# Kernel optimization log

Hardware: AMD Instinct MI355X
Metric: run time of the kernel (lower is better)

The kernel has to match this reference:

```python
import jax, jax.numpy as jnp
import numpy as np

THETA = 1.0
DILATIONS = (1, 2, 3, 4)
EPS = 1e-6


def _scale_features(x, d):
    # x: [B, C, H, W]; one pyramid scale (dilation d)
    B, C, H, W = x.shape
    k = 3 + 2 * (d - 1)          # kernel size per original formula
    pad = d * d                   # pad so effective span d*(k-1)+1 = 2d^2+1 preserves HxW
    K = k * k
    patches = jax.lax.conv_general_dilated_patches(
        x, (k, k), (1, 1), [(pad, pad), (pad, pad)], rhs_dilation=(d, d)
    )  # [B, C*K, H, W], channel-major per input channel
    p = patches.reshape(B, C, K, H, W)

    mu = p.mean(axis=2, keepdims=True)
    diff = p - mu
    var_biased = (diff * diff).mean(axis=2)                 # E[(p-mu)^2]
    std = jnp.sqrt(var_biased * (K / (K - 1))) + EPS        # torch .std is unbiased (ddof=1)

    contrast = var_biased / (std * std)                     # mean(normed^2)
    energy = (p * p).mean(axis=2)
    entropy = -(p * jnp.log(p + EPS)).mean(axis=2)
    # NB: original precedence -> 1.0 / mean(1 + |p - mu|)
    homogeneity = 1.0 / ((1.0 + jnp.abs(diff)).mean(axis=2))

    feats = jnp.stack([contrast, energy, entropy, homogeneity], axis=2)  # [B, C, 4, H, W]
    # martingale transform: exp(theta*log(f+eps) - 0.5*theta^2)
    M = jnp.exp(THETA * jnp.log(feats + EPS) - 0.5 * THETA ** 2)
    return M.reshape(B, C * 4, H, W)  # cat over channels of per-channel feature stacks


def setup_inputs() -> dict:
    key = jax.random.key(0)
    x = jax.random.uniform(key, (2, 4, 256, 256), dtype=jnp.float32)
    return {"x": x}


def reference(x):
    return tuple(_scale_features(x, d) for d in DILATIONS)
```

## Files before the change

### kernel.cpp

```cpp
#include <hip/hip_runtime.h>
#include <cstddef>

#define EPS 1e-6f
constexpr float INV_SQRT_E = 0.6065306597126334f;

template <int D>
__device__ __forceinline__ void body(const float* __restrict__ x,
                                     float* __restrict__ out,
                                     char* smem, int bc, int H, int W)
{
    constexpr int PAD = D * D;
    constexpr int KS  = 2 * D + 1;
    constexpr int K   = KS * KS;
    constexpr int TW  = 64, TH = 8;
    constexpr int LW  = TW + 2 * PAD;
    constexpr int LH  = TH + 2 * PAD;
    constexpr int NE  = LH * LW;
    constexpr int NI  = (NE + 511) / 512;
    constexpr float INVK = 1.0f / (float)K;
    constexpr float UNB  = (float)K / (float)(K - 1);

    float2* sv  = (float2*)smem;
    float2* cs2 = (float2*)(smem + LH * LW * 8);
    float*  cs1 = (float*) (smem + LH * LW * 8 + TH * LW * 8);

    const int w0 = blockIdx.x * TW;
    const int h0 = blockIdx.y * TH;
    const float* xp = x + (size_t)bc * H * W;
    const int tid = threadIdx.y * 64 + threadIdx.x;

    float vb[NI];
    #pragma unroll
    for (int i = 0; i < NI; ++i) {
        const int idx = tid + i * 512;
        float v = 0.0f;
        if (idx < NE) {
            const int r  = idx / LW;
            const int cc = idx - r * LW;
            const int gh = h0 - PAD + r;
            const int gw = w0 - PAD + cc;
            if (gh >= 0 && gh < H && gw >= 0 && gw < W) v = xp[gh * W + gw];
        }
        vb[i] = v;
    }
    #pragma unroll
    for (int i = 0; i < NI; ++i) {
        const int idx = tid + i * 512;
        if (idx < NE)
            sv[idx] = make_float2(vb[i], vb[i] * __logf(vb[i] + EPS));
    }
    __syncthreads();

    const int tx = threadIdx.x;
    const int ty = threadIdx.y;

    float s = 0.0f, s2 = 0.0f, sl = 0.0f;
    float sad;

    if constexpr (K <= 9) {
        const float2* base = &sv[ty * LW + tx];
        float ta[K];
        #pragma unroll
        for (int mi = 0; mi < KS; ++mi)
            #pragma unroll
            for (int mj = 0; mj < KS; ++mj) {
                const float2 p = base[(mi * D) * LW + mj * D];
                ta[mi * KS + mj] = p.x;
                s  += p.x;
                s2  = fmaf(p.x, p.x, s2);
                sl += p.y;
            }
        const float mu = s * INVK;
        sad = 0.0f;
        #pragma unroll
        for (int i = 0; i < K; ++i) sad += fabsf(ta[i] - mu);
    } else {
        constexpr int NC = TH * LW;
        for (int e = tid; e < NC; e += 512) {
            const int r = e / LW;
            const int c = e - r * LW;
            const float2* cp = &sv[r * LW + c];
            float vs = 0.0f, vs2 = 0.0f, vsl = 0.0f;
            #pragma unroll
            for (int mi = 0; mi < KS; ++mi) {
                const float2 p = cp[(mi * D) * LW];
                vs  += p.x;
                vs2  = fmaf(p.x, p.x, vs2);
                vsl += p.y;
            }
            cs2[e] = make_float2(vs, vs2);
            cs1[e] = vsl;
        }
        __syncthreads();

        const float2* q2 = &cs2[ty * LW + tx];
        const float*  q1 = &cs1[ty * LW + tx];
        #pragma unroll
        for (int mj = 0; mj < KS; ++mj) {
            const float2 q = q2[mj * D];
            s  += q.x;
            s2 += q.y;
            sl += q1[mj * D];
        }
        const float mu = s * INVK;

        const float2* base = &sv[ty * LW + tx];
        sad = 0.0f;
        #pragma unroll
        for (int mi = 0; mi < KS; ++mi)
            #pragma unroll
            for (int mj = 0; mj < KS; ++mj)
                sad += fabsf(base[(mi * D) * LW + mj * D].x - mu);
    }

    const float mu       = s * INVK;
    const float energy   = s2 * INVK;
    const float var      = fmaxf(energy - mu * mu, 0.0f);
    const float sd       = sqrtf(var * UNB) + EPS;
    const float contrast = var / (sd * sd);
    const float entropy  = -sl * INVK;
    const float homog    = 1.0f / (1.0f + sad * INVK);

    const size_t fstride = (size_t)H * W;
    const size_t rowoff  = (size_t)(h0 + ty) * W;
    float* op = out + (size_t)bc * 4 * fstride + w0 + tx;
    __builtin_nontemporal_store((contrast + EPS) * INV_SQRT_E, &op[0 * fstride + rowoff]);
    __builtin_nontemporal_store((energy   + EPS) * INV_SQRT_E, &op[1 * fstride + rowoff]);
    __builtin_nontemporal_store((entropy  + EPS) * INV_SQRT_E, &op[2 * fstride + rowoff]);
    __builtin_nontemporal_store((homog    + EPS) * INV_SQRT_E, &op[3 * fstride + rowoff]);
}

__global__ __launch_bounds__(512, 8) void tex_fused(
    const float* __restrict__ x, float* __restrict__ out, int H, int W)
{
    extern __shared__ char smem[];
    const int dz = blockIdx.z & 3;
    const int bc = blockIdx.z >> 2;
    const size_t per = (size_t)8 * 4 * H * W;
    switch (dz) {
        case 0: body<4>(x, out + 3 * per, smem, bc, H, W); break;
        case 1: body<3>(x, out + 2 * per, smem, bc, H, W); break;
        case 2: body<2>(x, out + 1 * per, smem, bc, H, W); break;
        default: body<1>(x, out + 0 * per, smem, bc, H, W); break;
    }
}

extern "C" void kernel_launch(void* const* d_in, const int* in_sizes, int n_in,
                              void* d_out, int out_size, void* d_ws, size_t ws_size,
                              hipStream_t stream) {
    const float* x = (const float*)d_in[0];
    float* out = (float*)d_out;

    const int H = 256, W = 256;
    const size_t smem_bytes = 39936;

    dim3 blk(64, 8, 1);
    dim3 grd(W / 64, H / 8, 8 * 4);
    tex_fused<<<grd, blk, smem_bytes, stream>>>(x, out, H, W);
}
```

Before: 79.88 us.

## Split shared tile into SoA arrays and share tap loads across paired output rows

The interleaved float2 shared-memory tile of (x, x·log x) becomes two separate float arrays, so passes that need only x no longer read the unused half. For dilations 2–4, each thread now computes column sums for two rows D apart, reusing the overlapping vertical taps. The absolute-deviation pass is restructured the same way: half the threads each compute SAD for a row pair, with row means exchanged through shared memory. This cuts LDS traffic in the dominant large-kernel passes, at the cost of extra barriers and leaving half the threads idle during the SAD stage.

```diff
diff --git a/kernel.cpp b/kernel.cpp
--- a/kernel.cpp
+++ b/kernel.cpp
@@ -20,9 +20,12 @@
     constexpr float INVK = 1.0f / (float)K;
     constexpr float UNB  = (float)K / (float)(K - 1);
 
-    float2* sv  = (float2*)smem;
-    float2* cs2 = (float2*)(smem + LH * LW * 8);
-    float*  cs1 = (float*) (smem + LH * LW * 8 + TH * LW * 8);
+    float*  sx  = (float*)smem;
+    float*  slg = sx + NE;
+    float2* cs2 = (float2*)(slg + NE);
+    float*  cs1 = (float*)(cs2 + TH * LW);
+    float*  muP  = (float*)cs2;
+    float*  sadP = muP + TH * 64;
 
     const int w0 = blockIdx.x * TW;
     const int h0 = blockIdx.y * TH;
@@ -46,94 +49,158 @@
     #pragma unroll
     for (int i = 0; i < NI; ++i) {
         const int idx = tid + i * 512;
-        if (idx < NE)
-            sv[idx] = make_float2(vb[i], vb[i] * __logf(vb[i] + EPS));
+        if (idx < NE) {
+            sx[idx]  = vb[i];
+            slg[idx] = vb[i] * __logf(vb[i] + EPS);
+        }
     }
     __syncthreads();
 
     const int tx = threadIdx.x;
     const int ty = threadIdx.y;
 
-    float s = 0.0f, s2 = 0.0f, sl = 0.0f;
-    float sad;
-
     if constexpr (K <= 9) {
-        const float2* base = &sv[ty * LW + tx];
-        float ta[K];
+        const float* bx = sx  + ty * LW + tx;
+        const float* bl = slg + ty * LW + tx;
+        float s = 0.f, s2 = 0.f, sl = 0.f, ta[K];
         #pragma unroll
         for (int mi = 0; mi < KS; ++mi)
             #pragma unroll
             for (int mj = 0; mj < KS; ++mj) {
-                const float2 p = base[(mi * D) * LW + mj * D];
-                ta[mi * KS + mj] = p.x;
-                s  += p.x;
-                s2  = fmaf(p.x, p.x, s2);
-                sl += p.y;
+                const float v = bx[mi * LW + mj];
+                ta[mi * KS + mj] = v;
+                s  += v;
+                s2  = fmaf(v, v, s2);
+                sl += bl[mi * LW + mj];
             }
         const float mu = s * INVK;
-        sad = 0.0f;
+        float sad = 0.f;
         #pragma unroll
         for (int i = 0; i < K; ++i) sad += fabsf(ta[i] - mu);
+
+        const float energy   = s2 * INVK;
+        const float var      = fmaxf(energy - mu * mu, 0.f);
+        const float sd       = sqrtf(var * UNB) + EPS;
+        const float contrast = var / (sd * sd);
+        const float entropy  = -sl * INVK;
+        const float homog    = 1.f / (1.f + sad * INVK);
+        const size_t fs = (size_t)H * W;
+        const size_t ro = (size_t)(h0 + ty) * W;
+        float* op = out + (size_t)bc * 4 * fs + w0 + tx;
+        __builtin_nontemporal_store((contrast + EPS) * INV_SQRT_E, &op[0 * fs + ro]);
+        __builtin_nontemporal_store((energy   + EPS) * INV_SQRT_E, &op[1 * fs + ro]);
+        __builtin_nontemporal_store((entropy  + EPS) * INV_SQRT_E, &op[2 * fs + ro]);
+        __builtin_nontemporal_store((homog    + EPS) * INV_SQRT_E, &op[3 * fs + ro]);
+        return;
     } else {
-        constexpr int NC = TH * LW;
-        for (int e = tid; e < NC; e += 512) {
-            const int r = e / LW;
-            const int c = e - r * LW;
-            const float2* cp = &sv[r * LW + c];
-            float vs = 0.0f, vs2 = 0.0f, vsl = 0.0f;
-            #pragma unroll
-            for (int mi = 0; mi < KS; ++mi) {
-                const float2 p = cp[(mi * D) * LW];
-                vs  += p.x;
-                vs2  = fmaf(p.x, p.x, vs2);
-                vsl += p.y;
+        for (int e = tid; e < 4 * LW; e += 512) {
+            const int p = e / LW;
+            const int c = e - p * LW;
+            const int vA = (D == 2) ? ((p < 2) ? p : p + 2) : p;
+            if (!(D == 3 && p == 3)) {
+                const int vB = vA + D;
+                const float* cx = sx  + vA * LW + c;
+                const float* cl = slg + vA * LW + c;
+                float sA = 0, qA = 0, lA = 0, sB = 0, qB = 0, lB = 0;
+                #pragma unroll
+                for (int t = 0; t <= KS; ++t) {
+                    const float v = cx[t * D * LW];
+                    const float g = cl[t * D * LW];
+                    if (t < KS)  { sA += v; qA = fmaf(v, v, qA); lA += g; }
+                    if (t >= 1)  { sB += v; qB = fmaf(v, v, qB); lB += g; }
+                }
+                cs2[vA * LW + c] = make_float2(sA, qA); cs1[vA * LW + c] = lA;
+                cs2[vB * LW + c] = make_float2(sB, qB); cs1[vB * LW + c] = lB;
+            } else {
+                #pragma unroll
+                for (int rr = 6; rr <= 7; ++rr) {
+                    const float* cx = sx  + rr * LW + c;
+                    const float* cl = slg + rr * LW + c;
+                    float s = 0, q = 0, l = 0;
+                    #pragma unroll
+                    for (int mi = 0; mi < KS; ++mi) {
+                        const float v = cx[mi * D * LW];
+                        s += v; q = fmaf(v, v, q); l += cl[mi * D * LW];
+                    }
+                    cs2[rr * LW + c] = make_float2(s, q); cs1[rr * LW + c] = l;
+                }
             }
-            cs2[e] = make_float2(vs, vs2);
-            cs1[e] = vsl;
-        }
-        __syncthreads();
-
-        const float2* q2 = &cs2[ty * LW + tx];
-        const float*  q1 = &cs1[ty * LW + tx];
+        }
+        __syncthreads();
+
+        float s = 0.f, s2 = 0.f, sl = 0.f;
+        const float2* q2 = cs2 + ty * LW + tx;
+        const float*  q1 = cs1 + ty * LW + tx;
         #pragma unroll
         for (int mj = 0; mj < KS; ++mj) {
             const float2 q = q2[mj * D];
-            s  += q.x;
-            s2 += q.y;
-            sl += q1[mj * D];
+            s += q.x; s2 += q.y; sl += q1[mj * D];
         }
         const float mu = s * INVK;
-
-        const float2* base = &sv[ty * LW + tx];
-        sad = 0.0f;
-        #pragma unroll
-        for (int mi = 0; mi < KS; ++mi)
-            #pragma unroll
-            for (int mj = 0; mj < KS; ++mj)
-                sad += fabsf(base[(mi * D) * LW + mj * D].x - mu);
-    }
-
-    const float mu       = s * INVK;
-    const float energy   = s2 * INVK;
-    const float var      = fmaxf(energy - mu * mu, 0.0f);
-    const float sd       = sqrtf(var * UNB) + EPS;
-    const float contrast = var / (sd * sd);
-    const float entropy  = -sl * INVK;
-    const float homog    = 1.0f / (1.0f + sad * INVK);
-
-    const size_t fstride = (size_t)H * W;
-    const size_t rowoff  = (size_t)(h0 + ty) * W;
-    float* op = out + (size_t)bc * 4 * fstride + w0 + tx;
-    __builtin_nontemporal_store((contrast + EPS) * INV_SQRT_E, &op[0 * fstride + rowoff]);
-    __builtin_nontemporal_store((energy   + EPS) * INV_SQRT_E, &op[1 * fstride + rowoff]);
-    __builtin_nontemporal_store((entropy  + EPS) * INV_SQRT_E, &op[2 * fstride + rowoff]);
-    __builtin_nontemporal_store((homog    + EPS) * INV_SQRT_E, &op[3 * fstride + rowoff]);
+        __syncthreads();
+
+        muP[ty * 64 + tx] = mu;
+        __syncthreads();
+
+        if (ty < 4) {
+            const int o = ty;
+            if (!(D == 3 && o == 3)) {
+                const int rA = (D == 2) ? ((o < 2) ? o : o + 2) : o;
+                const int rB = rA + D;
+                const float muA = muP[rA * 64 + tx];
+                const float muB = muP[rB * 64 + tx];
+                float sadA = 0.f, sadB = 0.f;
+                const float* bp = sx + rA * LW + tx;
+                #pragma unroll
+                for (int mj = 0; mj < KS; ++mj) {
+                    const float* cp = bp + mj * D;
+                    #pragma unroll
+                    for (int t = 0; t <= KS; ++t) {
+                        const float v = cp[t * D * LW];
+                        if (t < KS) sadA += fabsf(v - muA);
+                        if (t >= 1) sadB += fabsf(v - muB);
+                    }
+                }
+                sadP[rA * 64 + tx] = sadA;
+                sadP[rB * 64 + tx] = sadB;
+            } else {
+                #pragma unroll
+                for (int rr = 6; rr <= 7; ++rr) {
+                    const float mur = muP[rr * 64 + tx];
+                    const float* bp = sx + rr * LW + tx;
+                    float sd = 0.f;
+                    #pragma unroll
+                    for (int mi = 0; mi < KS; ++mi)
+                        #pragma unroll
+                        for (int mj = 0; mj < KS; ++mj)
+                            sd += fabsf(bp[mi * D * LW + mj * D] - mur);
+                    sadP[rr * 64 + tx] = sd;
+                }
+            }
+        }
+        __syncthreads();
+        const float sad = sadP[ty * 64 + tx];
+
+        const float energy   = s2 * INVK;
+        const float var      = fmaxf(energy - mu * mu, 0.f);
+        const float sd       = sqrtf(var * UNB) + EPS;
+        const float contrast = var / (sd * sd);
+        const float entropy  = -sl * INVK;
+        const float homog    = 1.f / (1.f + sad * INVK);
+        const size_t fs = (size_t)H * W;
+        const size_t ro = (size_t)(h0 + ty) * W;
+        float* op = out + (size_t)bc * 4 * fs + w0 + tx;
+        __builtin_nontemporal_store((contrast + EPS) * INV_SQRT_E, &op[0 * fs + ro]);
+        __builtin_nontemporal_store((energy   + EPS) * INV_SQRT_E, &op[1 * fs + ro]);
+        __builtin_nontemporal_store((entropy  + EPS) * INV_SQRT_E, &op[2 * fs + ro]);
+        __builtin_nontemporal_store((homog    + EPS) * INV_SQRT_E, &op[3 * fs + ro]);
+    }
 }
 
 __global__ __launch_bounds__(512, 8) void tex_fused(
     const float* __restrict__ x, float* __restrict__ out, int H, int W)
 {
-    extern __shared__ char smem[];
+    extern __shared__ __align__(16) char smem[];
     const int dz = blockIdx.z & 3;
     const int bc = blockIdx.z >> 2;
     const size_t per = (size_t)8 * 4 * H * W;
```

Result: faster. 77.49 us, median of 2 (-3.0%).
